# Performance work log

Measured on AMD Instinct MI355X. Metric: run time of the kernel, lower is better.

Reference implementation:

```python
import jax, jax.numpy as jnp
import numpy as np

N_HEADS = 16
SEG_LEN = 512
MSG_LEN = 1536
T_TOTAL = SEG_LEN + MSG_LEN  # 2048


def _build_mask(T):
    # rows < SEG_LEN: attend to all cols < SEG_LEN (full, non-causal block)
    # rows >= SEG_LEN: standard causal (cols <= row)
    rows = jnp.arange(T)[:, None]
    cols = jnp.arange(T)[None, :]
    mask = jnp.where(rows < SEG_LEN, cols < SEG_LEN, cols <= rows)
    return mask  # [T, T] bool


def setup_inputs() -> dict:
    key = jax.random.key(0)
    k1, k2, k3 = jax.random.split(key, 3)
    B, T, E = 4, T_TOTAL, 1024
    x = jax.random.normal(k1, (B, T, E), dtype=jnp.float32)
    W_qkv = jax.random.normal(k2, (E, 3 * E), dtype=jnp.float32) * (1.0 / np.sqrt(E))
    b_qkv = jnp.zeros((3 * E,), dtype=jnp.float32)
    W_proj = jax.random.normal(k3, (E, E), dtype=jnp.float32) * (1.0 / np.sqrt(E))
    b_proj = jnp.zeros((E,), dtype=jnp.float32)
    return {"x": x, "W_qkv": W_qkv, "b_qkv": b_qkv, "W_proj": W_proj, "b_proj": b_proj}


def reference(x, W_qkv, b_qkv, W_proj, b_proj):
    B, T, E = x.shape
    H = N_HEADS
    D = E // H
    qkv = x @ W_qkv + b_qkv  # [B, T, 3E]
    q, k, v = jnp.split(qkv, 3, axis=-1)
    # [B, H, T, D]
    q = q.reshape(B, T, H, D).transpose(0, 2, 1, 3)
    k = k.reshape(B, T, H, D).transpose(0, 2, 1, 3)
    v = v.reshape(B, T, H, D).transpose(0, 2, 1, 3)
    att = jnp.einsum("bhqd,bhkd->bhqk", q, k) * (1.0 / np.sqrt(D))
    mask = _build_mask(T)  # [T, T]
    att = jnp.where(mask[None, None], att, jnp.float32(-jnp.inf))
    att = jax.nn.softmax(att, axis=-1)
    y = jnp.einsum("bhqk,bhkd->bhqd", att, v)
    y = y.transpose(0, 2, 1, 3).reshape(B, T, E)
    return y @ W_proj + b_proj
```

## Files before the change

kernel.cpp:

```cpp
#include <hip/hip_runtime.h>


typedef _Float16 f16;
typedef _Float16 f16x4 __attribute__((ext_vector_type(4)));
typedef _Float16 f16x8 __attribute__((ext_vector_type(8)));
typedef float f32x4 __attribute__((ext_vector_type(4)));

#define MFMA16x32(a, b, c) __builtin_amdgcn_mfma_f32_16x16x32_f16(a, b, c, 0, 0, 0)
#define MFMA16x16(a, b, c) __builtin_amdgcn_mfma_f32_16x16x16f16(a, b, c, 0, 0, 0)

__device__ __forceinline__ void gload_lds16(const void* g, void* l) {
  __builtin_amdgcn_global_load_lds(
      (__attribute__((address_space(1))) void*)g,
      (__attribute__((address_space(3))) void*)l, 16, 0, 0);
}


__global__ void k_cast_f16(const float* __restrict__ x, f16* __restrict__ xh) {
  int i = blockIdx.x * 256 + threadIdx.x;
  float4 v = ((const float4*)x)[i];
  f16x4 o = {(f16)v.x, (f16)v.y, (f16)v.z, (f16)v.w};
  ((f16x4*)xh)[i] = o;
}

__global__ void k_transpose(const float* __restrict__ W, f16* __restrict__ Wt,
                            int Kdim, int Ndim) {
  __shared__ float tile[32][33];
  int n = blockIdx.x * 32 + threadIdx.x;
  int k0 = blockIdx.y * 32;
  for (int j = threadIdx.y; j < 32; j += 8)
    tile[j][threadIdx.x] = W[(size_t)(k0 + j) * Ndim + n];
  __syncthreads();
  int k = k0 + threadIdx.x;
  for (int j = threadIdx.y; j < 32; j += 8)
    Wt[(size_t)(blockIdx.x * 32 + j) * Kdim + k] = (f16)tile[threadIdx.x][j];
}


__global__ __launch_bounds__(256) void k_gemm_qkv(
    const f16* __restrict__ A, const f16* __restrict__ Bt,
    const float* __restrict__ bias,
    f16* __restrict__ Qo, f16* __restrict__ Ko, f16* __restrict__ Vo) {
  constexpr int KD = 1024;
  __shared__ __align__(16) f16 As[128 * 32];
  __shared__ __align__(16) f16 Bs[128 * 32];
  __shared__ __align__(16) f16 Esh[4 * 64 * 72];
  const int tid = threadIdx.x;
  const int wave = tid >> 6, lane = tid & 63;
  const int g = lane >> 4, l16 = lane & 15;
  const int m0 = blockIdx.y * 128, n0 = blockIdx.x * 128;
  const int wm = (wave >> 1) * 64, wn = (wave & 1) * 64;
  const int srow = wave * 16 + (lane >> 2);
  const int skc = (lane & 3) * 8;

  f32x4 acc[4][4] = {};

  for (int k0 = 0; k0 < KD; k0 += 32) {
    __syncthreads();
    for (int it = 0; it < 2; ++it) {
      gload_lds16(A + (size_t)(m0 + it * 64 + srow) * KD + k0 + skc,
                  As + (it * 64 + wave * 16) * 32);
      gload_lds16(Bt + (size_t)(n0 + it * 64 + srow) * KD + k0 + skc,
                  Bs + (it * 64 + wave * 16) * 32);
    }
    __syncthreads();
    f16x8 af[4], bf[4];
    for (int mi = 0; mi < 4; ++mi)
      af[mi] = *(const f16x8*)(As + (wm + mi * 16 + l16) * 32 + g * 8);
    for (int ni = 0; ni < 4; ++ni)
      bf[ni] = *(const f16x8*)(Bs + (wn + ni * 16 + l16) * 32 + g * 8);
    for (int mi = 0; mi < 4; ++mi)
      for (int ni = 0; ni < 4; ++ni)
        acc[mi][ni] = MFMA16x32(af[mi], bf[ni], acc[mi][ni]);
  }

  const int nsub = n0 + wn;
  const int part = nsub >> 10;
  const int h    = (nsub >> 6) & 15;
  const int mg   = m0 + wm;
  const int b    = mg >> 11;
  const int tb   = mg & 2047;
  const size_t bh = (size_t)(b * 16 + h);
  f16* Es = Esh + wave * (64 * 72);

  float bv[4];
  for (int ni = 0; ni < 4; ++ni) bv[ni] = bias[nsub + ni * 16 + l16];

  for (int mi = 0; mi < 4; ++mi)
    for (int ni = 0; ni < 4; ++ni)
      for (int r = 0; r < 4; ++r) {
        f16 hv = (f16)(acc[mi][ni][r] + bv[ni]);
        int mrow = mi * 16 + g * 4 + r, ncol = ni * 16 + l16;
        if (part == 2) Es[ncol * 72 + mrow] = hv;
        else           Es[mrow * 72 + ncol] = hv;
      }

  const int rrow = lane >> 3, rcol = (lane & 7) * 8;
  for (int p = 0; p < 8; ++p) {
    int row = p * 8 + rrow;
    f16x8 vv = *(const f16x8*)(Es + row * 72 + rcol);
    if (part == 0)
      *(f16x8*)(Qo + (bh * 2048 + tb + row) * 64 + rcol) = vv;
    else if (part == 1)
      *(f16x8*)(Ko + (bh * 2048 + tb + row) * 64 + rcol) = vv;
    else
      *(f16x8*)(Vo + (bh * 64 + row) * 2048 + tb + rcol) = vv;
  }
}


__constant__ unsigned char cQT[40] = {0, 1, 2,  3,  4,  4,  5,  5,  6,  6,
                                      7, 7, 8,  8,  8,  9,  9,  9,  10, 10,
                                      10, 11, 11, 11, 12, 12, 12, 12, 13, 13,
                                      13, 13, 14, 14, 14, 14, 15, 15, 15, 15};
__constant__ unsigned char cC0[40] = {0, 0, 0, 0,  0, 8, 0, 8, 0, 8,
                                      0, 8, 0, 8,  16, 0, 8, 16, 0, 8,
                                      16, 0, 8, 16, 0, 8, 16, 24, 0, 8,
                                      16, 24, 0, 8, 16, 24, 0, 8, 16, 24};

__global__ __launch_bounds__(256, 4) void k_attn(
    const f16* __restrict__ Q, const f16* __restrict__ Kb,
    const f16* __restrict__ Vt, float* __restrict__ Oacc,
    float* __restrict__ Rsum) {
  __shared__ __align__(16) f16 Ks[64 * 64];
  __shared__ __align__(16) f16 Vs[64 * 64];

  const int tid = threadIdx.x;
  const int wave = tid >> 6, lane = tid & 63;
  const int g = lane >> 4, l16 = lane & 15;
  const int bh = blockIdx.y;
  const int qt = cQT[blockIdx.x];
  const int c0 = cC0[blockIdx.x];
  const int q0 = qt * 128;
  const int nt = (qt < 4) ? 8 : (qt + 1) * 2;
  const int it_n = min(8, nt - c0);

  f16x8 aq[2][2];
  for (int mi = 0; mi < 2; ++mi) {
    const f16* qrow =
        Q + ((size_t)bh * 2048 + q0 + wave * 32 + mi * 16 + l16) * 64 + g * 8;
    aq[mi][0] = *(const f16x8*)(qrow);
    aq[mi][1] = *(const f16x8*)(qrow + 32);
    for (int kb = 0; kb < 2; ++kb)
      aq[mi][kb] = aq[mi][kb] * (f16)0.18033688f;
  }

  f32x4 o[2][4] = {};
  float rsum[2] = {};
  const int srowrel = lane >> 3;
  const int sc = (lane & 7) ^ srowrel;

  const f32x4 sinit = {-8.65617025f, -8.65617025f, -8.65617025f, -8.65617025f};

  for (int i = 0; i < it_n; ++i) {
    const int kt0 = (c0 + i) << 6;
    __syncthreads();
    for (int it = 0; it < 2; ++it) {
      int row = it * 32 + wave * 8 + srowrel;
      gload_lds16(Kb + ((size_t)bh * 2048 + kt0 + row) * 64 + sc * 8,
                  Ks + (it * 32 + wave * 8) * 64);
      gload_lds16(Vt + ((size_t)bh * 64 + row) * 2048 + kt0 + sc * 8,
                  Vs + (it * 32 + wave * 8) * 64);
    }
    __syncthreads();

    f32x4 t[2][4];
    for (int nb = 0; nb < 4; ++nb) {
      int R = nb * 16 + l16, sw = R & 7;
      f16x8 bk0 = *(const f16x8*)(Ks + R * 64 + ((0 + g) ^ sw) * 8);
      f16x8 bk1 = *(const f16x8*)(Ks + R * 64 + ((4 + g) ^ sw) * 8);
      for (int mi = 0; mi < 2; ++mi) {
        f32x4 acc = MFMA16x32(bk0, aq[mi][0], sinit);
        t[mi][nb] = MFMA16x32(bk1, aq[mi][1], acc);
      }
    }

    const bool masked = (q0 >= 512) && (kt0 >= q0);
    f16x4 ap[4][2];
    for (int mi = 0; mi < 2; ++mi) {
      const int mrow = q0 + wave * 32 + mi * 16 + l16;
      for (int nb = 0; nb < 4; ++nb)
        for (int r = 0; r < 4; ++r) {
          float p = __builtin_amdgcn_exp2f(t[mi][nb][r]);
          if (masked && (kt0 + nb * 16 + g * 4 + r > mrow)) p = 0.f;
          rsum[mi] += p;
          ap[nb][mi][r] = (f16)p;
        }
    }

    for (int db = 0; db < 4; ++db)
      for (int nb = 0; nb < 4; ++nb) {
        int R = db * 16 + l16, sw = R & 7;
        int c = nb * 2 + (g >> 1);
        f16x4 bv = *(const f16x4*)(Vs + R * 64 + (c ^ sw) * 8 + (g & 1) * 4);
        for (int mi = 0; mi < 2; ++mi)
          o[mi][db] = MFMA16x16(ap[nb][mi], bv, o[mi][db]);
      }
  }

  for (int mi = 0; mi < 2; ++mi) {
    rsum[mi] += __shfl_xor(rsum[mi], 16, 64);
    rsum[mi] += __shfl_xor(rsum[mi], 32, 64);
  }

  const size_t rowbase = (size_t)bh * 2048 + q0 + wave * 32;
  if (lane < 16)
    for (int mi = 0; mi < 2; ++mi)
      atomicAdd(&Rsum[rowbase + mi * 16 + l16], rsum[mi]);
  for (int mi = 0; mi < 2; ++mi)
    for (int db = 0; db < 4; ++db)
      for (int r = 0; r < 4; ++r)
        atomicAdd(&Oacc[(rowbase + mi * 16 + g * 4 + r) * 64 + db * 16 + l16],
                  o[mi][db][r]);
}


__global__ void k_combine(const float* __restrict__ Oacc,
                          const float* __restrict__ Rsum,
                          f16* __restrict__ Y) {
  int i = blockIdx.x * 256 + threadIdx.x;
  int d4 = i & 15;
  int t = (i >> 4) & 2047;
  int bh = i >> 15;
  float4 v = ((const float4*)Oacc)[i];
  float rinv = 1.0f / Rsum[(bh << 11) + t];
  int b = bh >> 4, h = bh & 15;
  f16x4 ov = {(f16)(v.x * rinv), (f16)(v.y * rinv), (f16)(v.z * rinv),
              (f16)(v.w * rinv)};
  *(f16x4*)(Y + ((size_t)(b * 2048 + t) * 1024 + h * 64 + d4 * 4)) = ov;
}


__global__ __launch_bounds__(256) void k_gemm_proj(
    const f16* __restrict__ A, const f16* __restrict__ Bt,
    const float* __restrict__ bias, float* __restrict__ out) {
  constexpr int KD = 1024;
  __shared__ __align__(16) f16 As[128 * 32];
  __shared__ __align__(16) f16 Bs[128 * 32];
  const int tid = threadIdx.x;
  const int wave = tid >> 6, lane = tid & 63;
  const int g = lane >> 4, l16 = lane & 15;
  const int m0 = blockIdx.y * 128, n0 = blockIdx.x * 128;
  const int wm = (wave >> 1) * 64, wn = (wave & 1) * 64;
  const int srow = wave * 16 + (lane >> 2);
  const int skc = (lane & 3) * 8;

  f32x4 acc[4][4] = {};

  for (int k0 = 0; k0 < KD; k0 += 32) {
    __syncthreads();
    for (int it = 0; it < 2; ++it) {
      gload_lds16(A + (size_t)(m0 + it * 64 + srow) * KD + k0 + skc,
                  As + (it * 64 + wave * 16) * 32);
      gload_lds16(Bt + (size_t)(n0 + it * 64 + srow) * KD + k0 + skc,
                  Bs + (it * 64 + wave * 16) * 32);
    }
    __syncthreads();
    f16x8 af[4], bf[4];
    for (int mi = 0; mi < 4; ++mi)
      af[mi] = *(const f16x8*)(As + (wm + mi * 16 + l16) * 32 + g * 8);
    for (int ni = 0; ni < 4; ++ni)
      bf[ni] = *(const f16x8*)(Bs + (wn + ni * 16 + l16) * 32 + g * 8);
    for (int mi = 0; mi < 4; ++mi)
      for (int ni = 0; ni < 4; ++ni)
        acc[mi][ni] = MFMA16x32(af[mi], bf[ni], acc[mi][ni]);
  }

  float bv[4];
  for (int ni = 0; ni < 4; ++ni) bv[ni] = bias[n0 + wn + ni * 16 + l16];

  for (int mi = 0; mi < 4; ++mi)
    for (int ni = 0; ni < 4; ++ni)
      for (int r = 0; r < 4; ++r) {
        int m = m0 + wm + mi * 16 + g * 4 + r;
        int n = n0 + wn + ni * 16 + l16;
        out[(size_t)m * 1024 + n] = acc[mi][ni][r] + bv[ni];
      }
}


extern "C" void kernel_launch(void* const* d_in, const int* in_sizes, int n_in,
                              void* d_out, int out_size, void* d_ws,
                              size_t ws_size, hipStream_t stream) {
  const float* x      = (const float*)d_in[0];
  const float* W_qkv  = (const float*)d_in[1];
  const float* b_qkv  = (const float*)d_in[2];
  const float* W_proj = (const float*)d_in[3];
  const float* b_proj = (const float*)d_in[4];
  float* out = (float*)d_out;

  char* ws = (char*)d_ws;
  f16* xh    = (f16*)ws;   ws += (size_t)8192 * 1024 * 2;
  f16* Wqt   = (f16*)ws;   ws += (size_t)3072 * 1024 * 2;
  f16* Wpt   = (f16*)ws;   ws += (size_t)1024 * 1024 * 2;
  f16* Qb    = (f16*)ws;   ws += (size_t)64 * 2048 * 64 * 2;
  f16* Kb    = (f16*)ws;   ws += (size_t)64 * 2048 * 64 * 2;
  f16* Vt    = (f16*)ws;   ws += (size_t)64 * 64 * 2048 * 2;
  float* Oacc = (float*)ws; ws += (size_t)64 * 2048 * 64 * 4;
  float* Rsum = (float*)ws; ws += (size_t)64 * 2048 * 4;
  f16* Y = xh;

  hipMemsetAsync(Oacc, 0, (size_t)64 * 2048 * 64 * 4 + (size_t)64 * 2048 * 4,
                 stream);

  k_cast_f16<<<8192, 256, 0, stream>>>(x, xh);
  k_transpose<<<dim3(96, 32), dim3(32, 8), 0, stream>>>(W_qkv, Wqt, 1024, 3072);
  k_transpose<<<dim3(32, 32), dim3(32, 8), 0, stream>>>(W_proj, Wpt, 1024, 1024);
  k_gemm_qkv<<<dim3(24, 64), 256, 0, stream>>>(xh, Wqt, b_qkv, Qb, Kb, Vt);
  k_attn<<<dim3(40, 64), 256, 0, stream>>>(Qb, Kb, Vt, Oacc, Rsum);
  k_combine<<<8192, 256, 0, stream>>>(Oacc, Rsum, Y);
  k_gemm_proj<<<dim3(8, 64), 256, 0, stream>>>(Y, Wpt, b_proj, out);
}
```

Measured before the change: 296.9 us.

## Fuse attention normalization into projection GEMM and reorder attention grid

Drops the separate combine kernel. The projection GEMM now reads the fp32 partial attention outputs and row sums directly, normalizes them and converts to f16 while staging its A tile into shared memory, which removes a full write and read of the intermediate Y tensor plus one launch. The attention grid is also transposed so that consecutive blocks cover different batch-heads at the same key/query chunk, changing block scheduling order and load balance. The cost is that the GEMM now does synchronous fp32 loads (twice the bytes, no async LDS load) and divisions in its main loop, and each fp32 element is re-read by every N-tile column block (eight times).

```diff
diff --git a/kernel.cpp b/kernel.cpp
--- a/kernel.cpp
+++ b/kernel.cpp
@@ -128,9 +128,9 @@
   const int tid = threadIdx.x;
   const int wave = tid >> 6, lane = tid & 63;
   const int g = lane >> 4, l16 = lane & 15;
-  const int bh = blockIdx.y;
-  const int qt = cQT[blockIdx.x];
-  const int c0 = cC0[blockIdx.x];
+  const int bh = blockIdx.x;
+  const int qt = cQT[blockIdx.y];
+  const int c0 = cC0[blockIdx.y];
   const int q0 = qt * 128;
   const int nt = (qt < 4) ? 8 : (qt + 1) * 2;
   const int it_n = min(8, nt - c0);
@@ -215,25 +215,10 @@
 }
 
 
-__global__ void k_combine(const float* __restrict__ Oacc,
-                          const float* __restrict__ Rsum,
-                          f16* __restrict__ Y) {
-  int i = blockIdx.x * 256 + threadIdx.x;
-  int d4 = i & 15;
-  int t = (i >> 4) & 2047;
-  int bh = i >> 15;
-  float4 v = ((const float4*)Oacc)[i];
-  float rinv = 1.0f / Rsum[(bh << 11) + t];
-  int b = bh >> 4, h = bh & 15;
-  f16x4 ov = {(f16)(v.x * rinv), (f16)(v.y * rinv), (f16)(v.z * rinv),
-              (f16)(v.w * rinv)};
-  *(f16x4*)(Y + ((size_t)(b * 2048 + t) * 1024 + h * 64 + d4 * 4)) = ov;
-}
-
-
 __global__ __launch_bounds__(256) void k_gemm_proj(
-    const f16* __restrict__ A, const f16* __restrict__ Bt,
-    const float* __restrict__ bias, float* __restrict__ out) {
+    const float* __restrict__ Oacc, const float* __restrict__ Rsum,
+    const f16* __restrict__ Bt, const float* __restrict__ bias,
+    float* __restrict__ out) {
   constexpr int KD = 1024;
   __shared__ __align__(16) f16 As[128 * 32];
   __shared__ __align__(16) f16 Bs[128 * 32];
@@ -244,14 +229,25 @@
   const int wm = (wave >> 1) * 64, wn = (wave & 1) * 64;
   const int srow = wave * 16 + (lane >> 2);
   const int skc = (lane & 3) * 8;
+  const int b = m0 >> 11;
 
   f32x4 acc[4][4] = {};
 
   for (int k0 = 0; k0 < KD; k0 += 32) {
+    const int h = k0 >> 6;
+    const int d0 = (k0 & 63) + skc;
     __syncthreads();
     for (int it = 0; it < 2; ++it) {
-      gload_lds16(A + (size_t)(m0 + it * 64 + srow) * KD + k0 + skc,
-                  As + (it * 64 + wave * 16) * 32);
+      int t = (m0 & 2047) + it * 64 + srow;
+      const float* op =
+          Oacc + ((size_t)(b * 16 + h) * 2048 + t) * 64 + d0;
+      float4 v0 = *(const float4*)(op);
+      float4 v1 = *(const float4*)(op + 4);
+      float rinv = 1.0f / Rsum[(size_t)(b * 16 + h) * 2048 + t];
+      f16x8 w = {(f16)(v0.x * rinv), (f16)(v0.y * rinv), (f16)(v0.z * rinv),
+                 (f16)(v0.w * rinv), (f16)(v1.x * rinv), (f16)(v1.y * rinv),
+                 (f16)(v1.z * rinv), (f16)(v1.w * rinv)};
+      *(f16x8*)(As + (it * 64 + srow) * 32 + skc) = w;
       gload_lds16(Bt + (size_t)(n0 + it * 64 + srow) * KD + k0 + skc,
                   Bs + (it * 64 + wave * 16) * 32);
     }
@@ -298,7 +294,6 @@
   f16* Vt    = (f16*)ws;   ws += (size_t)64 * 64 * 2048 * 2;
   float* Oacc = (float*)ws; ws += (size_t)64 * 2048 * 64 * 4;
   float* Rsum = (float*)ws; ws += (size_t)64 * 2048 * 4;
-  f16* Y = xh;
 
   hipMemsetAsync(Oacc, 0, (size_t)64 * 2048 * 64 * 4 + (size_t)64 * 2048 * 4,
                  stream);
@@ -307,7 +302,6 @@
   k_transpose<<<dim3(96, 32), dim3(32, 8), 0, stream>>>(W_qkv, Wqt, 1024, 3072);
   k_transpose<<<dim3(32, 32), dim3(32, 8), 0, stream>>>(W_proj, Wpt, 1024, 1024);
   k_gemm_qkv<<<dim3(24, 64), 256, 0, stream>>>(xh, Wqt, b_qkv, Qb, Kb, Vt);
-  k_attn<<<dim3(40, 64), 256, 0, stream>>>(Qb, Kb, Vt, Oacc, Rsum);
-  k_combine<<<8192, 256, 0, stream>>>(Oacc, Rsum, Y);
-  k_gemm_proj<<<dim3(8, 64), 256, 0, stream>>>(Y, Wpt, b_proj, out);
-}
+  k_attn<<<dim3(64, 40), 256, 0, stream>>>(Qb, Kb, Vt, Oacc, Rsum);
+  k_gemm_proj<<<dim3(8, 64), 256, 0, stream>>>(Oacc, Rsum, Wpt, b_proj, out);
+}
```

Result: no change. 298.1 us (+0.4%).
